# Optimization experiments

Hardware: AMD Instinct MI355X
Metric: run time of the kernel (lower is better)

Reference implementation:

```python
import jax, jax.numpy as jnp
import numpy as np

INV_L_MIN, INV_L_MAX = 0.5, 2.0

def _gelu(x):
    return jax.nn.gelu(x, approximate=False)

def _scaled_sigmoid(x, lo, hi):
    return lo + (hi - lo) * jax.nn.sigmoid(x)

def _fourier_bases(nodes, modes):
    # nodes: [b, n, d]; modes: [k, d, w] -> temp: [b, n, k, w]
    temp = 2.0 * jnp.pi * jnp.einsum('bxd,kdw->bxkw', nodes, modes)
    return jnp.cos(temp), jnp.sin(temp), jnp.ones_like(temp[:, :, :1, :])

def _spectral_conv(x, wc, ws, w0, bc, bs, b0, wbc, wbs, wb0):
    # x: [b, c_in, n]; forward non-uniform Fourier transform via weighted bases
    x_c = jnp.einsum('bix,bxkw->bikw', x, wbc)
    x_s = -jnp.einsum('bix,bxkw->bikw', x, wbs)
    x_0 = jnp.einsum('bix,bxkw->bikw', x, wb0)
    f_c = jnp.einsum('bikw,iokw->bokw', x_c, wc) - jnp.einsum('bikw,iokw->bokw', x_s, ws)
    f_s = jnp.einsum('bikw,iokw->bokw', x_s, wc) + jnp.einsum('bikw,iokw->bokw', x_c, ws)
    f_0 = jnp.einsum('bikw,iokw->bokw', x_0, w0)
    return (jnp.einsum('bokw,bxkw->box', f_0, b0)
            + 2.0 * jnp.einsum('bokw,bxkw->box', f_c, bc)
            - 2.0 * jnp.einsum('bokw,bxkw->box', f_s, bs))


def setup_inputs() -> dict:
    key = jax.random.key(0)
    ks = jax.random.split(key, 32)
    B, NU, NV = 4, 65536, 16384
    K, D, W = 32, 2, 1          # nmodes, ndims, nmeasures
    C, L = 64, 3                # channels, number of BNO layers
    FC, IU, IV, OUT = 128, 2, 3, 1
    f32 = jnp.float32
    rn = lambda k, s, sc=1.0: (sc * jax.random.normal(k, s, dtype=f32))
    ru = lambda k, s, sc=1.0: (sc * jax.random.uniform(k, s, dtype=f32))
    sp_scale = 1.0 / (C * C)
    inp = {
        'u': rn(ks[0], (B, NU, IU)),
        'v': rn(ks[1], (B, NV, IV)),
        'node_mask_u': jnp.ones((B, NU, 1), dtype=jnp.int32),
        'nodes_u': ru(ks[2], (B, NU, D)),
        'nodes_v': ru(ks[3], (B, NV, D)),
        'node_weights_u': ru(ks[4], (B, NU, W), 1.0 / NU),
        'node_weights_v': ru(ks[5], (B, NV, W), 1.0 / NV),
        'modes': ru(ks[6], (K, D, W), 8.0),
        # scaled_logit(1.0, 0.5, 2.0) = log((1-0.5)/(2-1)) = log(0.5)
        'inv_L_scale_latent': jnp.full((D, W), -0.69314718, dtype=f32),
        'fc0_u_w': rn(ks[7], (C, IU), 0.5), 'fc0_u_b': rn(ks[8], (C,), 0.1),
        'fc0_v_w': rn(ks[9], (C, IV), 0.5), 'fc0_v_b': rn(ks[10], (C,), 0.1),
        'sp_ext_wc': ru(ks[11], (L, C, C, K, W), sp_scale),
        'sp_ext_ws': ru(ks[12], (L, C, C, K, W), sp_scale),
        'sp_ext_w0': ru(ks[13], (L, C, C, 1, W), sp_scale),
        'sp_u_wc': ru(ks[14], (L, C, C, K, W), sp_scale),
        'sp_u_ws': ru(ks[15], (L, C, C, K, W), sp_scale),
        'sp_u_w0': ru(ks[16], (L, C, C, 1, W), sp_scale),
        'sp_v_wc': ru(ks[17], (L, C, C, K, W), sp_scale),
        'sp_v_ws': ru(ks[18], (L, C, C, K, W), sp_scale),
        'sp_v_w0': ru(ks[19], (L, C, C, 1, W), sp_scale),
        'ws_u_w': rn(ks[20], (L, C, C), 0.05), 'ws_u_b': rn(ks[21], (L, C), 0.02),
        'ws_v_w': rn(ks[22], (L, C, C), 0.05), 'ws_v_b': rn(ks[23], (L, C), 0.02),
        'fc1_w': rn(ks[24], (FC, C), 0.05), 'fc1_b': rn(ks[25], (FC,), 0.02),
        'fc2_w': rn(ks[26], (OUT, FC), 0.05), 'fc2_b': rn(ks[27], (OUT,), 0.02),
    }
    return inp


def reference(u, v, node_mask_u, nodes_u, nodes_v, node_weights_u, node_weights_v,
              modes, inv_L_scale_latent, fc0_u_w, fc0_u_b, fc0_v_w, fc0_v_b,
              sp_ext_wc, sp_ext_ws, sp_ext_w0, sp_u_wc, sp_u_ws, sp_u_w0,
              sp_v_wc, sp_v_ws, sp_v_w0, ws_u_w, ws_u_b, ws_v_w, ws_v_b,
              fc1_w, fc1_b, fc2_w, fc2_b):
    # node_mask_u is unpacked but unused in the original forward
    m = modes * _scaled_sigmoid(inv_L_scale_latent, INV_L_MIN, INV_L_MAX)  # [k,d,w]
    bc_u, bs_u, b0_u = _fourier_bases(nodes_u, m)
    bc_v, bs_v, b0_v = _fourier_bases(nodes_v, m)
    wu = node_weights_u[:, :, None, :]  # [b,x,1,w]
    wv = node_weights_v[:, :, None, :]
    wbc_u, wbs_u, wb0_u = bc_u * wu, bs_u * wu, b0_u * wu
    wbc_v, wbs_v, wb0_v = bc_v * wv, bs_v * wv, b0_v * wv
    # lift to channel dim and move to [b, c, n]
    u = jnp.einsum('bxi,oi->box', u, fc0_u_w) + fc0_u_b[None, :, None]
    v = jnp.einsum('bxi,oi->box', v, fc0_v_w) + fc0_v_b[None, :, None]
    L = ws_u_w.shape[0]
    for i in range(L):
        u1 = _spectral_conv(v, sp_ext_wc[i], sp_ext_ws[i], sp_ext_w0[i],
                            bc_u, bs_u, b0_u, wbc_v, wbs_v, wb0_v)
        u2 = _spectral_conv(u, sp_u_wc[i], sp_u_ws[i], sp_u_w0[i],
                            bc_u, bs_u, b0_u, wbc_u, wbs_u, wb0_u)
        u3 = jnp.einsum('oi,bix->box', ws_u_w[i], u) + ws_u_b[i][None, :, None]
        u = u1 + u2 + u3
        if i != L - 1:  # v is only updated on non-final layers, as in the original
            u = _gelu(u)
            v1 = _spectral_conv(v, sp_v_wc[i], sp_v_ws[i], sp_v_w0[i],
                                bc_v, bs_v, b0_v, wbc_v, wbs_v, wb0_v)
            v2 = jnp.einsum('oi,bix->box', ws_v_w[i], v) + ws_v_b[i][None, :, None]
            v = _gelu(v1 + v2)
    u = jnp.transpose(u, (0, 2, 1))  # [b, n, c]
    u = _gelu(u @ fc1_w.T + fc1_b)
    return u @ fc2_w.T + fc2_b
```

## Files before the change

### kernel.cpp

```cpp
#include <hip/hip_runtime.h>
#include <math.h>

#define PI2 6.283185307179586f

typedef __attribute__((ext_vector_type(8))) short bf16x8;
typedef __attribute__((ext_vector_type(4))) float f32x4;

__device__ __forceinline__ float gelu_f(float x) {
    return 0.5f * x * (1.0f + erff(x * 0.7071067811865476f));
}
__device__ __forceinline__ unsigned short f2bf(float f) {
    unsigned int u = __float_as_uint(f);
    u += 0x7FFFu + ((u >> 16) & 1u);
    return (unsigned short)(u >> 16);
}
__device__ __forceinline__ float bf2f(unsigned short h) {
    return __uint_as_float(((unsigned int)h) << 16);
}
__device__ __forceinline__ unsigned int pk(unsigned short a, unsigned short b) {
    return (unsigned int)a | ((unsigned int)b << 16);
}
__device__ __forceinline__ void wsplit(float w, unsigned short* dst) {
    unsigned short h = f2bf(w);
    dst[0] = h;
    dst[128] = f2bf(w - bf2f(h));
}

template<int NIN>
__global__ __launch_bounds__(256) void k_prep(const float* __restrict__ nodes, const float* __restrict__ modes,
                                              const float* __restrict__ latent, const float* __restrict__ nw,
                                              const float* __restrict__ inp, const float* __restrict__ fcw,
                                              const float* __restrict__ fcb,
                                              unsigned short* __restrict__ FTb, unsigned short* __restrict__ ch0,
                                              unsigned short* __restrict__ wbb,
                                              unsigned short* __restrict__ part, int N) {
    int b = blockIdx.y;
    int tid = threadIdx.x;
    int xl = tid & 127, half = tid >> 7;
    int x = blockIdx.x * 128 + xl;
    __shared__ unsigned short st_c[64][136];
    __shared__ unsigned short st_w[65][136];
    float s0 = 0.5f + 1.5f / (1.0f + expf(-latent[0]));
    float s1 = 0.5f + 1.5f / (1.0f + expf(-latent[1]));
    float n0 = nodes[((size_t)b * N + x) * 2 + 0];
    float n1 = nodes[((size_t)b * N + x) * 2 + 1];
    float wx = nw[(size_t)b * N + x];
    unsigned short* wb = wbb + (size_t)b * 65 * N + x;
    unsigned int fcos[8], fsin[8], fch[16];
    #pragma unroll
    for (int kk = 0; kk < 16; ++kk) {
        int k = half * 16 + kk;
        float m0 = modes[k * 2 + 0] * s0;
        float m1 = modes[k * 2 + 1] * s1;
        float t = PI2 * (n0 * m0 + n1 * m1);
        float s, c;
        sincosf(t, &s, &c);
        unsigned short hc = f2bf(c), hs = f2bf(s);
        if (kk & 1) { fcos[kk >> 1] |= ((unsigned int)hc << 16); fsin[kk >> 1] |= ((unsigned int)hs << 16); }
        else        { fcos[kk >> 1] = hc;                         fsin[kk >> 1] = hs; }
        unsigned short hcw = f2bf(c * wx), hsw = f2bf(s * wx);
        st_w[k][xl] = hcw;
        st_w[32 + k][xl] = hsw;
        wb[(size_t)k * N] = hcw;
        wb[(size_t)(32 + k) * N] = hsw;
    }
    if (half) {
        unsigned short hw = f2bf(wx);
        st_w[64][xl] = hw;
        wb[(size_t)64 * N] = hw;
    }
    float xi[NIN];
    #pragma unroll
    for (int i = 0; i < NIN; ++i) xi[i] = inp[((size_t)b * N + x) * NIN + i];
    #pragma unroll
    for (int cc = 0; cc < 32; ++cc) {
        int c = half * 32 + cc;
        float a = fcb[c];
        #pragma unroll
        for (int i = 0; i < NIN; ++i) a += fcw[c * NIN + i] * xi[i];
        unsigned short h = f2bf(a);
        st_c[c][xl] = h;
        if (cc & 1) fch[cc >> 1] |= ((unsigned int)h << 16);
        else fch[cc >> 1] = h;
    }
    unsigned int* fr = (unsigned int*)(FTb + ((size_t)b * N + x) * 64);
    #pragma unroll
    for (int i = 0; i < 8; ++i) fr[half * 8 + i] = fcos[i];
    #pragma unroll
    for (int i = 0; i < 8; ++i) fr[16 + half * 8 + i] = fsin[i];
    unsigned int* cr = (unsigned int*)(ch0 + ((size_t)b * N + x) * 64);
    #pragma unroll
    for (int i = 0; i < 16; ++i) cr[half * 16 + i] = fch[i];
    __syncthreads();
    int lane = tid & 63, wv = tid >> 6;
    int lm = lane & 15, lg = lane >> 4;
    int ro = wv * 16;
    f32x4 acc[5] = {};
    #pragma unroll
    for (int xs = 0; xs < 128; xs += 32) {
        bf16x8 a = *(const bf16x8*)&st_c[ro + lm][xs + lg * 8];
        #pragma unroll
        for (int ct = 0; ct < 4; ++ct) {
            bf16x8 bw = *(const bf16x8*)&st_w[ct * 16 + lm][xs + lg * 8];
            acc[ct] = __builtin_amdgcn_mfma_f32_16x16x32_bf16(a, bw, acc[ct], 0, 0, 0);
        }
        bf16x8 wf = *(const bf16x8*)&st_w[64][xs + lg * 8];
        acc[4] = __builtin_amdgcn_mfma_f32_16x16x32_bf16(a, wf, acc[4], 0, 0, 0);
    }
    unsigned short* pb = part + (size_t)(b * (N / 128) + blockIdx.x) * 64 * 66;
    #pragma unroll
    for (int ct = 0; ct < 4; ++ct)
        #pragma unroll
        for (int j = 0; j < 4; ++j)
            pb[(ro + lg * 4 + j) * 66 + ct * 16 + lm] = f2bf(acc[ct][j]);
    if (lm == 0) {
        #pragma unroll
        for (int j = 0; j < 4; ++j) pb[(ro + lg * 4 + j) * 66 + 64] = f2bf(acc[4][j]);
    }
}

__global__ __launch_bounds__(256) void k_reduce2(const unsigned short* __restrict__ part_u,
                                                 const unsigned short* __restrict__ part_v,
                                                 float* __restrict__ momu, float* __restrict__ momv,
                                                 int chu, int chv, int B_) {
    int by = blockIdx.y;
    const unsigned short* p;
    float* m;
    int nch, b;
    if (by < B_) { b = by; p = part_u; m = momu; nch = chu; }
    else { b = by - B_; p = part_v; m = momv; nch = chv; }
    int eg = threadIdx.x >> 3;
    int sp = threadIdx.x & 7;
    int e = blockIdx.x * 32 + eg;
    __shared__ float red[32][8];
    float s = 0.f;
    int row = 0, col = 0;
    if (e < 64 * 65) {
        row = e / 65; col = e % 65;
        const unsigned short* pp = p + ((size_t)(b * nch) * 64 + row) * 66 + col;
        for (int c = sp; c < nch; c += 8)
            s += bf2f(pp[(size_t)c * 64 * 66]);
    }
    red[eg][sp] = s;
    __syncthreads();
    if (sp == 0 && e < 64 * 65) {
        float t = 0.f;
        #pragma unroll
        for (int i = 0; i < 8; ++i) t += red[eg][i];
        m[((size_t)b * 64 + row) * 66 + col] = t;
    }
}

__global__ __launch_bounds__(256) void k_tw(const float* __restrict__ e_c, const float* __restrict__ e_s,
                                            const float* __restrict__ u_c, const float* __restrict__ u_s,
                                            const float* __restrict__ v_c, const float* __restrict__ v_s,
                                            float* __restrict__ oT) {
    int li = blockIdx.x;
    int a = blockIdx.y;
    const float* in;
    switch (a) {
        case 0: in = e_c; break;
        case 1: in = e_s; break;
        case 2: in = u_c; break;
        case 3: in = u_s; break;
        case 4: in = v_c; break;
        default: in = v_s; break;
    }
    float* outp = oT + (size_t)a * 393216;
    int l = li >> 6, i = li & 63;
    __shared__ float t[32][65];
    int tid = threadIdx.x;
    const float* ib = in + (size_t)l * 131072 + (size_t)i * 2048;
    #pragma unroll
    for (int r = 0; r < 8; ++r) {
        int e = r * 256 + tid;
        t[e & 31][e >> 5] = ib[e];
    }
    __syncthreads();
    float* ob = outp + (size_t)l * 131072 + (size_t)i * 64;
    #pragma unroll
    for (int r = 0; r < 8; ++r) {
        int e = r * 256 + tid;
        ob[(size_t)(e >> 6) * 4096 + (e & 63)] = t[e >> 6][e & 63];
    }
}

__global__ void k_buildW(const float* __restrict__ momu, const float* __restrict__ momv,
                         const float* __restrict__ ecT, const float* __restrict__ esT, const float* __restrict__ ew0,
                         const float* __restrict__ ucT, const float* __restrict__ usT, const float* __restrict__ uw0,
                         const float* __restrict__ vcT, const float* __restrict__ vsT, const float* __restrict__ vw0,
                         const float* __restrict__ wsuw, const float* __restrict__ wsub,
                         const float* __restrict__ wsvw, const float* __restrict__ wsvb,
                         unsigned short* __restrict__ WuBf, unsigned short* __restrict__ WvBf,
                         float* __restrict__ biasU, float* __restrict__ biasV, int do_v) {
    int b = blockIdx.y, j = blockIdx.x, o = threadIdx.x;
    const float* mu = momu + (size_t)b * 64 * 66;
    const float* mv = momv + (size_t)b * 64 * 66;
    unsigned short* Wub = WuBf + ((size_t)b * 64 + o) * 256;
    unsigned short* Wvb = WvBf + ((size_t)b * 64 + o) * 256;
    if (j < 32) {
        int k = j;
        const float* ec = ecT + (size_t)k * 4096;
        const float* es = esT + (size_t)k * 4096;
        const float* uc = ucT + (size_t)k * 4096;
        const float* us = usT + (size_t)k * 4096;
        const float* vc = vcT + (size_t)k * 4096;
        const float* vs = vsT + (size_t)k * 4096;
        float fcu = 0, fsu = 0, fcv = 0, fsv = 0;
        for (int i = 0; i < 64; ++i) {
            float Scv = mv[i * 66 + k], Ssv = mv[i * 66 + 32 + k];
            float Scu = mu[i * 66 + k], Ssu = mu[i * 66 + 32 + k];
            int wi = i * 64 + o;
            float e_c = ec[wi], e_s = es[wi];
            float u_c = uc[wi], u_s = us[wi];
            fcu += Scv * e_c + Ssv * e_s + Scu * u_c + Ssu * u_s;
            fsu += Scv * e_s - Ssv * e_c + Scu * u_s - Ssu * u_c;
            if (do_v) {
                float v_c = vc[wi], v_s = vs[wi];
                fcv += Scv * v_c + Ssv * v_s;
                fsv += Scv * v_s - Ssv * v_c;
            }
        }
        wsplit(2.f * fcu, Wub + k);
        wsplit(-2.f * fsu, Wub + 32 + k);
        if (do_v) {
            wsplit(2.f * fcv, Wvb + k);
            wsplit(-2.f * fsv, Wvb + 32 + k);
        }
    } else {
        for (int c = 0; c < 64; ++c) wsplit(wsuw[o * 64 + c], Wub + 64 + c);
        float f0u = 0;
        for (int i = 0; i < 64; ++i)
            f0u += mv[i * 66 + 64] * ew0[i * 64 + o] + mu[i * 66 + 64] * uw0[i * 64 + o];
        biasU[b * 64 + o] = f0u + wsub[o];
        if (do_v) {
            for (int c = 0; c < 64; ++c) wsplit(wsvw[o * 64 + c], Wvb + 64 + c);
            float f0v = 0;
            for (int i = 0; i < 64; ++i) f0v += mv[i * 66 + 64] * vw0[i * 64 + o];
            biasV[b * 64 + o] = f0v + wsvb[o];
        }
    }
}

__global__ void k_buildW_slow(const float* __restrict__ momu, const float* __restrict__ momv,
                              const float* __restrict__ ewc, const float* __restrict__ ews, const float* __restrict__ ew0,
                              const float* __restrict__ uwc, const float* __restrict__ uws, const float* __restrict__ uw0,
                              const float* __restrict__ vwc, const float* __restrict__ vws, const float* __restrict__ vw0,
                              const float* __restrict__ wsuw, const float* __restrict__ wsub,
                              const float* __restrict__ wsvw, const float* __restrict__ wsvb,
                              unsigned short* __restrict__ WuBf, unsigned short* __restrict__ WvBf,
                              float* __restrict__ biasU, float* __restrict__ biasV, int do_v) {
    int b = blockIdx.y, j = blockIdx.x, o = threadIdx.x;
    const float* mu = momu + (size_t)b * 64 * 66;
    const float* mv = momv + (size_t)b * 64 * 66;
    unsigned short* Wub = WuBf + ((size_t)b * 64 + o) * 256;
    unsigned short* Wvb = WvBf + ((size_t)b * 64 + o) * 256;
    if (j < 32) {
        int k = j;
        float fcu = 0, fsu = 0, fcv = 0, fsv = 0;
        for (int i = 0; i < 64; ++i) {
            float Scv = mv[i * 66 + k], Ssv = mv[i * 66 + 32 + k];
            float Scu = mu[i * 66 + k], Ssu = mu[i * 66 + 32 + k];
            int wi = (i * 64 + o) * 32 + k;
            float ec = ewc[wi], es = ews[wi];
            float uc = uwc[wi], us = uws[wi];
            fcu += Scv * ec + Ssv * es + Scu * uc + Ssu * us;
            fsu += Scv * es - Ssv * ec + Scu * us - Ssu * uc;
            if (do_v) {
                float vc = vwc[wi], vs = vws[wi];
                fcv += Scv * vc + Ssv * vs;
                fsv += Scv * vs - Ssv * vc;
            }
        }
        wsplit(2.f * fcu, Wub + k);
        wsplit(-2.f * fsu, Wub + 32 + k);
        if (do_v) {
            wsplit(2.f * fcv, Wvb + k);
            wsplit(-2.f * fsv, Wvb + 32 + k);
        }
    } else {
        for (int c = 0; c < 64; ++c) wsplit(wsuw[o * 64 + c], Wub + 64 + c);
        float f0u = 0;
        for (int i = 0; i < 64; ++i)
            f0u += mv[i * 66 + 64] * ew0[i * 64 + o] + mu[i * 66 + 64] * uw0[i * 64 + o];
        biasU[b * 64 + o] = f0u + wsub[o];
        if (do_v) {
            for (int c = 0; c < 64; ++c) wsplit(wsvw[o * 64 + c], Wvb + 64 + c);
            float f0v = 0;
            for (int i = 0; i < 64; ++i) f0v += mv[i * 66 + 64] * vw0[i * 64 + o];
            biasV[b * 64 + o] = f0v + wsvb[o];
        }
    }
}

__global__ __launch_bounds__(256, 2) void k_synth3(const unsigned short* __restrict__ WuBf,
                                                   const unsigned short* __restrict__ WvBf,
                                                   const float* __restrict__ biasU, const float* __restrict__ biasV,
                                                   const unsigned short* __restrict__ FTb_u,
                                                   const unsigned short* __restrict__ FTb_v,
                                                   const unsigned short* __restrict__ chIn_u,
                                                   const unsigned short* __restrict__ chIn_v,
                                                   unsigned short* __restrict__ chOut_u,
                                                   unsigned short* __restrict__ chOut_v,
                                                   const unsigned short* __restrict__ wbb_u,
                                                   const unsigned short* __restrict__ wbb_v,
                                                   unsigned short* __restrict__ part_u, unsigned short* __restrict__ part_v,
                                                   int NU_, int NV_, int nbu, int act_u, int wch_v) {
    int bx = blockIdx.x, b = blockIdx.y, tid = threadIdx.x;
    const unsigned short *Wb, *FTb, *chIn, *wb;
    const float* bi;
    unsigned short *chOut, *pb;
    int N, act, wch, blk;
    if (bx < nbu) {
        blk = bx; Wb = WuBf; bi = biasU; FTb = FTb_u; chIn = chIn_u; chOut = chOut_u; N = NU_;
        wb = wbb_u + (size_t)b * 65 * NU_;
        pb = part_u + (size_t)(b * (NU_ / 128) + blk) * 64 * 66;
        act = act_u; wch = 1;
    } else {
        blk = bx - nbu; Wb = WvBf; bi = biasV; FTb = FTb_v; chIn = chIn_v; chOut = chOut_v; N = NV_;
        wb = wbb_v + (size_t)b * 65 * NV_;
        pb = part_v + (size_t)(b * (NV_ / 128) + blk) * 64 * 66;
        act = 1; wch = wch_v;
    }
    int lane = tid & 63, wv = tid >> 6;
    int lm = lane & 15, lg = lane >> 4;
    int ro = wv * 16;
    int r0 = ro + lg * 4;
    int x0 = blk * 128;
    bf16x8 wfr[4][5];
    #pragma unroll
    for (int xi = 0; xi < 4; ++xi) {
        int xs = xi * 32;
        #pragma unroll
        for (int ct = 0; ct < 4; ++ct)
            wfr[xi][ct] = *(const bf16x8*)(wb + (size_t)(ct * 16 + lm) * N + x0 + xs + lg * 8);
        wfr[xi][4] = *(const bf16x8*)(wb + (size_t)64 * N + x0 + xs + lg * 8);
    }
    const unsigned short* Wrow = Wb + ((size_t)b * 64 + ro + lm) * 256;
    bf16x8 ahi[4], alo[4];
    #pragma unroll
    for (int kt = 0; kt < 4; ++kt) {
        ahi[kt] = *(const bf16x8*)(Wrow + kt * 32 + lg * 8);
        alo[kt] = *(const bf16x8*)(Wrow + 128 + kt * 32 + lg * 8);
    }
    float bias[4];
    #pragma unroll
    for (int j = 0; j < 4; ++j) bias[j] = bi[b * 64 + ro + lg * 4 + j];
    const unsigned short* fbb = FTb + (size_t)b * N * 64;
    const unsigned short* cib = chIn + (size_t)b * N * 64;
    unsigned short* cob = chOut + (size_t)b * N * 64;
    __shared__ unsigned short st2[64][136];
    f32x4 acc[8] = {};
    #pragma unroll
    for (int hh = 0; hh < 2; ++hh) {
        bf16x8 bfr[4][4];
        #pragma unroll
        for (int xt = 0; xt < 4; ++xt) {
            size_t xr = (size_t)(x0 + (hh * 4 + xt) * 16 + lm) * 64 + lg * 8;
            bfr[xt][0] = *(const bf16x8*)(fbb + xr);
            bfr[xt][1] = *(const bf16x8*)(fbb + xr + 32);
            bfr[xt][2] = *(const bf16x8*)(cib + xr);
            bfr[xt][3] = *(const bf16x8*)(cib + xr + 32);
        }
        #pragma unroll
        for (int xt = 0; xt < 4; ++xt)
            #pragma unroll
            for (int kt = 0; kt < 4; ++kt) {
                acc[hh * 4 + xt] = __builtin_amdgcn_mfma_f32_16x16x32_bf16(ahi[kt], bfr[xt][kt], acc[hh * 4 + xt], 0, 0, 0);
                acc[hh * 4 + xt] = __builtin_amdgcn_mfma_f32_16x16x32_bf16(alo[kt], bfr[xt][kt], acc[hh * 4 + xt], 0, 0, 0);
            }
    }
    #pragma unroll
    for (int xt = 0; xt < 8; ++xt) {
        int xl = xt * 16 + lm;
        float v[4];
        #pragma unroll
        for (int j = 0; j < 4; ++j) {
            v[j] = acc[xt][j] + bias[j];
            if (act) v[j] = gelu_f(v[j]);
        }
        unsigned short h[4];
        #pragma unroll
        for (int j = 0; j < 4; ++j) h[j] = f2bf(v[j]);
        st2[r0 + 0][xl] = h[0];
        st2[r0 + 1][xl] = h[1];
        st2[r0 + 2][xl] = h[2];
        st2[r0 + 3][xl] = h[3];
        if (wch) {
            unsigned int* dst = (unsigned int*)(cob + (size_t)(x0 + xl) * 64 + r0);
            dst[0] = pk(h[0], h[1]);
            dst[1] = pk(h[2], h[3]);
        }
    }
    __syncthreads();
    f32x4 macc[5] = {};
    #pragma unroll
    for (int xi = 0; xi < 4; ++xi) {
        int xs = xi * 32;
        bf16x8 a = *(const bf16x8*)&st2[ro + lm][xs + lg * 8];
        #pragma unroll
        for (int ct = 0; ct < 4; ++ct)
            macc[ct] = __builtin_amdgcn_mfma_f32_16x16x32_bf16(a, wfr[xi][ct], macc[ct], 0, 0, 0);
        macc[4] = __builtin_amdgcn_mfma_f32_16x16x32_bf16(a, wfr[xi][4], macc[4], 0, 0, 0);
    }
    #pragma unroll
    for (int ct = 0; ct < 4; ++ct)
        #pragma unroll
        for (int j = 0; j < 4; ++j)
            pb[(r0 + j) * 66 + ct * 16 + lm] = f2bf(macc[ct][j]);
    if (lm == 0) {
        #pragma unroll
        for (int j = 0; j < 4; ++j) pb[(r0 + j) * 66 + 64] = f2bf(macc[4][j]);
    }
}

__global__ __launch_bounds__(256, 2) void k_synthfc(const unsigned short* __restrict__ WuBf,
                                                    const float* __restrict__ biasU,
                                                    const unsigned short* __restrict__ FTb_u,
                                                    const unsigned short* __restrict__ chIn_u,
                                                    const float* __restrict__ w1, const float* __restrict__ b1,
                                                    const float* __restrict__ w2, const float* __restrict__ b2,
                                                    float* __restrict__ out, int N) {
    int blk = blockIdx.x, b = blockIdx.y, tid = threadIdx.x;
    int lane = tid & 63, wv = tid >> 6;
    int lm = lane & 15, lg = lane >> 4;
    int ro = wv * 16;
    int r0 = ro + lg * 4;
    int x0 = blk * 128;
    int f0 = wv * 32;
    float wtmp[2][2][8];
    #pragma unroll
    for (int ft = 0; ft < 2; ++ft)
        #pragma unroll
        for (int kt = 0; kt < 2; ++kt) {
            const float* wp = w1 + (size_t)(f0 + ft * 16 + lm) * 64 + kt * 32 + lg * 8;
            *(float4*)&wtmp[ft][kt][0] = *(const float4*)wp;
            *(float4*)&wtmp[ft][kt][4] = *(const float4*)(wp + 4);
        }
    const unsigned short* Wrow = WuBf + ((size_t)b * 64 + ro + lm) * 256;
    bf16x8 ahi[4], alo[4];
    #pragma unroll
    for (int kt = 0; kt < 4; ++kt) {
        ahi[kt] = *(const bf16x8*)(Wrow + kt * 32 + lg * 8);
        alo[kt] = *(const bf16x8*)(Wrow + 128 + kt * 32 + lg * 8);
    }
    float bias[4];
    #pragma unroll
    for (int j = 0; j < 4; ++j) bias[j] = biasU[b * 64 + ro + lg * 4 + j];
    const unsigned short* fbb = FTb_u + (size_t)b * N * 64;
    const unsigned short* cib = chIn_u + (size_t)b * N * 64;
    __shared__ unsigned short st2t[128][72];
    __shared__ float red[4][8][16];
    f32x4 acc[8] = {};
    #pragma unroll
    for (int hh = 0; hh < 2; ++hh) {
        bf16x8 bfr[4][4];
        #pragma unroll
        for (int xt = 0; xt < 4; ++xt) {
            size_t xr = (size_t)(x0 + (hh * 4 + xt) * 16 + lm) * 64 + lg * 8;
            bfr[xt][0] = *(const bf16x8*)(fbb + xr);
            bfr[xt][1] = *(const bf16x8*)(fbb + xr + 32);
            bfr[xt][2] = *(const bf16x8*)(cib + xr);
            bfr[xt][3] = *(const bf16x8*)(cib + xr + 32);
        }
        #pragma unroll
        for (int xt = 0; xt < 4; ++xt)
            #pragma unroll
            for (int kt = 0; kt < 4; ++kt) {
                acc[hh * 4 + xt] = __builtin_amdgcn_mfma_f32_16x16x32_bf16(ahi[kt], bfr[xt][kt], acc[hh * 4 + xt], 0, 0, 0);
                acc[hh * 4 + xt] = __builtin_amdgcn_mfma_f32_16x16x32_bf16(alo[kt], bfr[xt][kt], acc[hh * 4 + xt], 0, 0, 0);
            }
    }
    #pragma unroll
    for (int xt = 0; xt < 8; ++xt) {
        int xl = xt * 16 + lm;
        float v0 = acc[xt][0] + bias[0];
        float v1 = acc[xt][1] + bias[1];
        float v2 = acc[xt][2] + bias[2];
        float v3 = acc[xt][3] + bias[3];
        *(unsigned int*)&st2t[xl][r0] = pk(f2bf(v0), f2bf(v1));
        *(unsigned int*)&st2t[xl][r0 + 2] = pk(f2bf(v2), f2bf(v3));
    }
    __syncthreads();
    bf16x8 whi[2][2], wlo[2][2];
    #pragma unroll
    for (int ft = 0; ft < 2; ++ft)
        #pragma unroll
        for (int kt = 0; kt < 2; ++kt)
            #pragma unroll
            for (int i = 0; i < 8; ++i) {
                unsigned short h = f2bf(wtmp[ft][kt][i]);
                whi[ft][kt][i] = (short)h;
                wlo[ft][kt][i] = (short)f2bf(wtmp[ft][kt][i] - bf2f(h));
            }
    float b1v[2][4], w2v[2][4];
    #pragma unroll
    for (int ft = 0; ft < 2; ++ft)
        #pragma unroll
        for (int j = 0; j < 4; ++j) {
            int f = f0 + ft * 16 + lg * 4 + j;
            b1v[ft][j] = b1[f];
            w2v[ft][j] = w2[f];
        }
    f32x4 facc[8][2] = {};
    #pragma unroll
    for (int xt = 0; xt < 8; ++xt) {
        int xl = xt * 16 + lm;
        bf16x8 bf0 = *(const bf16x8*)&st2t[xl][lg * 8];
        bf16x8 bf1 = *(const bf16x8*)&st2t[xl][32 + lg * 8];
        #pragma unroll
        for (int ft = 0; ft < 2; ++ft) {
            facc[xt][ft] = __builtin_amdgcn_mfma_f32_16x16x32_bf16(whi[ft][0], bf0, facc[xt][ft], 0, 0, 0);
            facc[xt][ft] = __builtin_amdgcn_mfma_f32_16x16x32_bf16(wlo[ft][0], bf0, facc[xt][ft], 0, 0, 0);
            facc[xt][ft] = __builtin_amdgcn_mfma_f32_16x16x32_bf16(whi[ft][1], bf1, facc[xt][ft], 0, 0, 0);
            facc[xt][ft] = __builtin_amdgcn_mfma_f32_16x16x32_bf16(wlo[ft][1], bf1, facc[xt][ft], 0, 0, 0);
        }
    }
    #pragma unroll
    for (int xt = 0; xt < 8; ++xt) {
        float s = 0.f;
        #pragma unroll
        for (int ft = 0; ft < 2; ++ft)
            #pragma unroll
            for (int j = 0; j < 4; ++j) {
                float v = facc[xt][ft][j] + b1v[ft][j];
                s += w2v[ft][j] * gelu_f(v);
            }
        s += __shfl_xor(s, 16, 64);
        s += __shfl_xor(s, 32, 64);
        if (lg == 0) red[wv][xt][lm] = s;
    }
    __syncthreads();
    if (tid < 128) {
        int xt = tid >> 4, lmm = tid & 15;
        float s = b2[0] + red[0][xt][lmm] + red[1][xt][lmm] + red[2][xt][lmm] + red[3][xt][lmm];
        out[(size_t)b * N + x0 + tid] = s;
    }
}

extern "C" void kernel_launch(void* const* d_in, const int* in_sizes, int n_in,
                              void* d_out, int out_size, void* d_ws, size_t ws_size,
                              hipStream_t stream) {
    const float* u_in = (const float*)d_in[0];
    const float* v_in = (const float*)d_in[1];
    const float* nodes_u = (const float*)d_in[3];
    const float* nodes_v = (const float*)d_in[4];
    const float* nwu = (const float*)d_in[5];
    const float* nwv = (const float*)d_in[6];
    const float* modes = (const float*)d_in[7];
    const float* latent = (const float*)d_in[8];
    const float* fc0uw = (const float*)d_in[9];
    const float* fc0ub = (const float*)d_in[10];
    const float* fc0vw = (const float*)d_in[11];
    const float* fc0vb = (const float*)d_in[12];
    const float* ewc = (const float*)d_in[13];
    const float* ews = (const float*)d_in[14];
    const float* ew0 = (const float*)d_in[15];
    const float* uwc = (const float*)d_in[16];
    const float* uws = (const float*)d_in[17];
    const float* uw0 = (const float*)d_in[18];
    const float* vwc = (const float*)d_in[19];
    const float* vws = (const float*)d_in[20];
    const float* vw0 = (const float*)d_in[21];
    const float* wsuw = (const float*)d_in[22];
    const float* wsub = (const float*)d_in[23];
    const float* wsvw = (const float*)d_in[24];
    const float* wsvb = (const float*)d_in[25];
    const float* fc1w = (const float*)d_in[26];
    const float* fc1b = (const float*)d_in[27];
    const float* fc2w = (const float*)d_in[28];
    const float* fc2b = (const float*)d_in[29];
    float* out = (float*)d_out;

    const int B = 4, NU = 65536, NV = 16384;
    const int CH_U = NU / 128, CH_V = NV / 128;

    unsigned short* FTb_u = (unsigned short*)d_ws;
    unsigned short* FTb_v = FTb_u + (size_t)B * NU * 64;
    unsigned short* chU0 = FTb_v + (size_t)B * NV * 64;
    unsigned short* chU1 = chU0 + (size_t)B * NU * 64;
    unsigned short* chV0 = chU1 + (size_t)B * NU * 64;
    unsigned short* chV1 = chV0 + (size_t)B * NV * 64;
    unsigned short* wbb_u = chV1 + (size_t)B * NV * 64;
    unsigned short* wbb_v = wbb_u + (size_t)B * 65 * NU;
    unsigned short* part_u = wbb_v + (size_t)B * 65 * NV;
    unsigned short* part_v = part_u + (size_t)B * CH_U * 64 * 66;
    float* momu = (float*)(part_v + (size_t)B * CH_V * 64 * 66);
    float* momv = momu + B * 64 * 66;
    unsigned short* WuBf = (unsigned short*)(momv + B * 64 * 66);
    unsigned short* WvBf = WuBf + (size_t)B * 64 * 256;
    float* biasU = (float*)(WvBf + (size_t)B * 64 * 256);
    float* biasV = biasU + B * 64;
    float* wT = biasV + B * 64;
    size_t need_T = (size_t)((char*)(wT + 6 * 393216) - (char*)d_ws);
    int use_T = (ws_size >= need_T) ? 1 : 0;

    k_prep<2><<<dim3(NU / 128, B), 256, 0, stream>>>(nodes_u, modes, latent, nwu, u_in, fc0uw, fc0ub,
                                                     FTb_u, chU0, wbb_u, part_u, NU);
    k_prep<3><<<dim3(NV / 128, B), 256, 0, stream>>>(nodes_v, modes, latent, nwv, v_in, fc0vw, fc0vb,
                                                     FTb_v, chV0, wbb_v, part_v, NV);
    if (use_T)
        k_tw<<<dim3(192, 6), 256, 0, stream>>>(ewc, ews, uwc, uws, vwc, vws, wT);

    for (int l = 0; l < 3; ++l) {
        int do_v = (l < 2) ? 1 : 0;
        k_reduce2<<<dim3(130, 2 * B), 256, 0, stream>>>(part_u, part_v, momu, momv, CH_U, CH_V, B);
        if (use_T) {
            k_buildW<<<dim3(33, B), 64, 0, stream>>>(momu, momv,
                wT + 0 * 393216 + l * 131072, wT + 1 * 393216 + l * 131072, ew0 + (size_t)l * 64 * 64,
                wT + 2 * 393216 + l * 131072, wT + 3 * 393216 + l * 131072, uw0 + (size_t)l * 64 * 64,
                wT + 4 * 393216 + l * 131072, wT + 5 * 393216 + l * 131072, vw0 + (size_t)l * 64 * 64,
                wsuw + l * 64 * 64, wsub + l * 64, wsvw + l * 64 * 64, wsvb + l * 64,
                WuBf, WvBf, biasU, biasV, do_v);
        } else {
            k_buildW_slow<<<dim3(33, B), 64, 0, stream>>>(momu, momv,
                ewc + (size_t)l * 64 * 64 * 32, ews + (size_t)l * 64 * 64 * 32, ew0 + (size_t)l * 64 * 64,
                uwc + (size_t)l * 64 * 64 * 32, uws + (size_t)l * 64 * 64 * 32, uw0 + (size_t)l * 64 * 64,
                vwc + (size_t)l * 64 * 64 * 32, vws + (size_t)l * 64 * 64 * 32, vw0 + (size_t)l * 64 * 64,
                wsuw + l * 64 * 64, wsub + l * 64, wsvw + l * 64 * 64, wsvb + l * 64,
                WuBf, WvBf, biasU, biasV, do_v);
        }
        if (l < 2) {
            int nbu = NU / 128;
            int nbx = nbu + NV / 128;
            const unsigned short* chInU = (l & 1) ? chU1 : chU0;
            unsigned short* chOutU = (l & 1) ? chU0 : chU1;
            const unsigned short* chInV = (l & 1) ? chV1 : chV0;
            unsigned short* chOutV = (l & 1) ? chV0 : chV1;
            int wch_v = (l == 0) ? 1 : 0;
            k_synth3<<<dim3(nbx, B), 256, 0, stream>>>(WuBf, WvBf, biasU, biasV,
                                                       FTb_u, FTb_v, chInU, chInV, chOutU, chOutV,
                                                       wbb_u, wbb_v, part_u, part_v,
                                                       NU, NV, nbu, 1 , wch_v);
        } else {
            k_synthfc<<<dim3(NU / 128, B), 256, 0, stream>>>(WuBf, biasU, FTb_u, chU0,
                                                             fc1w, fc1b, fc2w, fc2b, out, NU);
        }
    }
}
```

Before: 446.5 us.

## Replace per-block partial moments and reduce kernel with float atomics into ping-pong buffers

```diff
diff --git a/kernel.cpp b/kernel.cpp
--- a/kernel.cpp
+++ b/kernel.cpp
@@ -33,7 +33,7 @@
                                               const float* __restrict__ fcb,
                                               unsigned short* __restrict__ FTb, unsigned short* __restrict__ ch0,
                                               unsigned short* __restrict__ wbb,
-                                              unsigned short* __restrict__ part, int N) {
+                                              float* __restrict__ mom, int N) {
     int b = blockIdx.y;
     int tid = threadIdx.x;
     int xl = tid & 127, half = tid >> 7;
@@ -107,47 +107,15 @@
         bf16x8 wf = *(const bf16x8*)&st_w[64][xs + lg * 8];
         acc[4] = __builtin_amdgcn_mfma_f32_16x16x32_bf16(a, wf, acc[4], 0, 0, 0);
     }
-    unsigned short* pb = part + (size_t)(b * (N / 128) + blockIdx.x) * 64 * 66;
+    float* mb = mom + (size_t)b * 64 * 66;
     #pragma unroll
     for (int ct = 0; ct < 4; ++ct)
         #pragma unroll
         for (int j = 0; j < 4; ++j)
-            pb[(ro + lg * 4 + j) * 66 + ct * 16 + lm] = f2bf(acc[ct][j]);
+            atomicAdd(&mb[(ro + lg * 4 + j) * 66 + ct * 16 + lm], acc[ct][j]);
     if (lm == 0) {
         #pragma unroll
-        for (int j = 0; j < 4; ++j) pb[(ro + lg * 4 + j) * 66 + 64] = f2bf(acc[4][j]);
-    }
-}
-
-__global__ __launch_bounds__(256) void k_reduce2(const unsigned short* __restrict__ part_u,
-                                                 const unsigned short* __restrict__ part_v,
-                                                 float* __restrict__ momu, float* __restrict__ momv,
-                                                 int chu, int chv, int B_) {
-    int by = blockIdx.y;
-    const unsigned short* p;
-    float* m;
-    int nch, b;
-    if (by < B_) { b = by; p = part_u; m = momu; nch = chu; }
-    else { b = by - B_; p = part_v; m = momv; nch = chv; }
-    int eg = threadIdx.x >> 3;
-    int sp = threadIdx.x & 7;
-    int e = blockIdx.x * 32 + eg;
-    __shared__ float red[32][8];
-    float s = 0.f;
-    int row = 0, col = 0;
-    if (e < 64 * 65) {
-        row = e / 65; col = e % 65;
-        const unsigned short* pp = p + ((size_t)(b * nch) * 64 + row) * 66 + col;
-        for (int c = sp; c < nch; c += 8)
-            s += bf2f(pp[(size_t)c * 64 * 66]);
-    }
-    red[eg][sp] = s;
-    __syncthreads();
-    if (sp == 0 && e < 64 * 65) {
-        float t = 0.f;
-        #pragma unroll
-        for (int i = 0; i < 8; ++i) t += red[eg][i];
-        m[((size_t)b * 64 + row) * 66 + col] = t;
+        for (int j = 0; j < 4; ++j) atomicAdd(&mb[(ro + lg * 4 + j) * 66 + 64], acc[4][j]);
     }
 }
 
@@ -304,22 +272,23 @@
                                                    unsigned short* __restrict__ chOut_v,
                                                    const unsigned short* __restrict__ wbb_u,
                                                    const unsigned short* __restrict__ wbb_v,
-                                                   unsigned short* __restrict__ part_u, unsigned short* __restrict__ part_v,
+                                                   float* __restrict__ momN_u, float* __restrict__ momN_v,
                                                    int NU_, int NV_, int nbu, int act_u, int wch_v) {
     int bx = blockIdx.x, b = blockIdx.y, tid = threadIdx.x;
     const unsigned short *Wb, *FTb, *chIn, *wb;
     const float* bi;
-    unsigned short *chOut, *pb;
+    unsigned short* chOut;
+    float* momN;
     int N, act, wch, blk;
     if (bx < nbu) {
         blk = bx; Wb = WuBf; bi = biasU; FTb = FTb_u; chIn = chIn_u; chOut = chOut_u; N = NU_;
         wb = wbb_u + (size_t)b * 65 * NU_;
-        pb = part_u + (size_t)(b * (NU_ / 128) + blk) * 64 * 66;
+        momN = momN_u;
         act = act_u; wch = 1;
     } else {
         blk = bx - nbu; Wb = WvBf; bi = biasV; FTb = FTb_v; chIn = chIn_v; chOut = chOut_v; N = NV_;
         wb = wbb_v + (size_t)b * 65 * NV_;
-        pb = part_v + (size_t)(b * (NV_ / 128) + blk) * 64 * 66;
+        momN = momN_v;
         act = 1; wch = wch_v;
     }
     int lane = tid & 63, wv = tid >> 6;
@@ -403,14 +372,15 @@
             macc[ct] = __builtin_amdgcn_mfma_f32_16x16x32_bf16(a, wfr[xi][ct], macc[ct], 0, 0, 0);
         macc[4] = __builtin_amdgcn_mfma_f32_16x16x32_bf16(a, wfr[xi][4], macc[4], 0, 0, 0);
     }
+    float* mb = momN + (size_t)b * 64 * 66;
     #pragma unroll
     for (int ct = 0; ct < 4; ++ct)
         #pragma unroll
         for (int j = 0; j < 4; ++j)
-            pb[(r0 + j) * 66 + ct * 16 + lm] = f2bf(macc[ct][j]);
+            atomicAdd(&mb[(r0 + j) * 66 + ct * 16 + lm], macc[ct][j]);
     if (lm == 0) {
         #pragma unroll
-        for (int j = 0; j < 4; ++j) pb[(r0 + j) * 66 + 64] = f2bf(macc[4][j]);
+        for (int j = 0; j < 4; ++j) atomicAdd(&mb[(r0 + j) * 66 + 64], macc[4][j]);
     }
 }
 
@@ -573,7 +543,7 @@
     float* out = (float*)d_out;
 
     const int B = 4, NU = 65536, NV = 16384;
-    const int CH_U = NU / 128, CH_V = NV / 128;
+    const size_t MOMSZ = (size_t)B * 64 * 66;
 
     unsigned short* FTb_u = (unsigned short*)d_ws;
     unsigned short* FTb_v = FTb_u + (size_t)B * NU * 64;
@@ -583,11 +553,9 @@
     unsigned short* chV1 = chV0 + (size_t)B * NV * 64;
     unsigned short* wbb_u = chV1 + (size_t)B * NV * 64;
     unsigned short* wbb_v = wbb_u + (size_t)B * 65 * NU;
-    unsigned short* part_u = wbb_v + (size_t)B * 65 * NV;
-    unsigned short* part_v = part_u + (size_t)B * CH_U * 64 * 66;
-    float* momu = (float*)(part_v + (size_t)B * CH_V * 64 * 66);
-    float* momv = momu + B * 64 * 66;
-    unsigned short* WuBf = (unsigned short*)(momv + B * 64 * 66);
+    float* momA = (float*)(wbb_v + (size_t)B * 65 * NV);
+    float* momB = momA + 2 * MOMSZ;
+    unsigned short* WuBf = (unsigned short*)(momB + 2 * MOMSZ);
     unsigned short* WvBf = WuBf + (size_t)B * 64 * 256;
     float* biasU = (float*)(WvBf + (size_t)B * 64 * 256);
     float* biasV = biasU + B * 64;
@@ -595,25 +563,27 @@
     size_t need_T = (size_t)((char*)(wT + 6 * 393216) - (char*)d_ws);
     int use_T = (ws_size >= need_T) ? 1 : 0;
 
+    hipMemsetAsync(momA, 0, 2 * MOMSZ * sizeof(float), stream);
     k_prep<2><<<dim3(NU / 128, B), 256, 0, stream>>>(nodes_u, modes, latent, nwu, u_in, fc0uw, fc0ub,
-                                                     FTb_u, chU0, wbb_u, part_u, NU);
+                                                     FTb_u, chU0, wbb_u, momA , NU);
     k_prep<3><<<dim3(NV / 128, B), 256, 0, stream>>>(nodes_v, modes, latent, nwv, v_in, fc0vw, fc0vb,
-                                                     FTb_v, chV0, wbb_v, part_v, NV);
+                                                     FTb_v, chV0, wbb_v, momA + MOMSZ , NV);
     if (use_T)
         k_tw<<<dim3(192, 6), 256, 0, stream>>>(ewc, ews, uwc, uws, vwc, vws, wT);
 
     for (int l = 0; l < 3; ++l) {
         int do_v = (l < 2) ? 1 : 0;
-        k_reduce2<<<dim3(130, 2 * B), 256, 0, stream>>>(part_u, part_v, momu, momv, CH_U, CH_V, B);
+        float* momCur = (l & 1) ? momB : momA;
+        float* momNext = (l & 1) ? momA : momB;
         if (use_T) {
-            k_buildW<<<dim3(33, B), 64, 0, stream>>>(momu, momv,
+            k_buildW<<<dim3(33, B), 64, 0, stream>>>(momCur, momCur + MOMSZ,
                 wT + 0 * 393216 + l * 131072, wT + 1 * 393216 + l * 131072, ew0 + (size_t)l * 64 * 64,
                 wT + 2 * 393216 + l * 131072, wT + 3 * 393216 + l * 131072, uw0 + (size_t)l * 64 * 64,
                 wT + 4 * 393216 + l * 131072, wT + 5 * 393216 + l * 131072, vw0 + (size_t)l * 64 * 64,
                 wsuw + l * 64 * 64, wsub + l * 64, wsvw + l * 64 * 64, wsvb + l * 64,
                 WuBf, WvBf, biasU, biasV, do_v);
         } else {
-            k_buildW_slow<<<dim3(33, B), 64, 0, stream>>>(momu, momv,
+            k_buildW_slow<<<dim3(33, B), 64, 0, stream>>>(momCur, momCur + MOMSZ,
                 ewc + (size_t)l * 64 * 64 * 32, ews + (size_t)l * 64 * 64 * 32, ew0 + (size_t)l * 64 * 64,
                 uwc + (size_t)l * 64 * 64 * 32, uws + (size_t)l * 64 * 64 * 32, uw0 + (size_t)l * 64 * 64,
                 vwc + (size_t)l * 64 * 64 * 32, vws + (size_t)l * 64 * 64 * 32, vw0 + (size_t)l * 64 * 64,
@@ -621,6 +591,7 @@
                 WuBf, WvBf, biasU, biasV, do_v);
         }
         if (l < 2) {
+            hipMemsetAsync(momNext, 0, 2 * MOMSZ * sizeof(float), stream);
             int nbu = NU / 128;
             int nbx = nbu + NV / 128;
             const unsigned short* chInU = (l & 1) ? chU1 : chU0;
@@ -630,7 +601,7 @@
             int wch_v = (l == 0) ? 1 : 0;
             k_synth3<<<dim3(nbx, B), 256, 0, stream>>>(WuBf, WvBf, biasU, biasV,
                                                        FTb_u, FTb_v, chInU, chInV, chOutU, chOutV,
-                                                       wbb_u, wbb_v, part_u, part_v,
+                                                       wbb_u, wbb_v, momNext, momNext + MOMSZ,
                                                        NU, NV, nbu, 1 , wch_v);
         } else {
             k_synthfc<<<dim3(NU / 128, B), 256, 0, stream>>>(WuBf, biasU, FTb_u, chU0,
```

New measurement: 647.7 us. 45.1% more time.
